# Kernel tuning notes

Hardware: AMD Instinct MI355X
Metric: run time of the kernel (lower is better)

Reference implementation:

```python
import jax, jax.numpy as jnp
import numpy as np

K = 20  # neighbors, per get_u_xt default


def setup_inputs() -> dict:
    key = jax.random.key(0)
    ks = jax.random.split(key, 6)
    B, N, D, H = 2048, 100000, 64, 256
    return {
        "t": jax.random.uniform(ks[0], (1,), dtype=jnp.float32),
        "z": jax.random.normal(ks[1], (B, D + 2), dtype=jnp.float32),
        "data": jax.random.normal(ks[2], (N, D), dtype=jnp.float32),
        "velocity": jax.random.normal(ks[3], (N, D), dtype=jnp.float32),
        "W1": jax.random.normal(ks[4], (D + 1, H), dtype=jnp.float32) * 0.05,
        "b1": jnp.zeros((H,), dtype=jnp.float32),
        "W2": jax.random.normal(ks[5], (H, D), dtype=jnp.float32) * 0.05,
        "b2": jnp.zeros((D,), dtype=jnp.float32),
    }


def _get_u_xt(xt, x, v, k=K):
    # Euclidean cdist via ||a||^2 + ||b||^2 - 2 a.b  -> [B, N]
    sq = (jnp.sum(xt * xt, axis=1)[:, None]
          + jnp.sum(x * x, axis=1)[None, :]
          - 2.0 * (xt @ x.T))
    dists = jnp.sqrt(jnp.maximum(sq, 1e-30))
    neg_d, knn_idx = jax.lax.top_k(-dists, k)  # k smallest distances
    knn_dists = -neg_d                          # ascending order, [B, k]
    h = jnp.maximum(knn_dists[:, -1:], 1e-12)   # bandwidth = k-th NN dist
    w = jnp.exp(-knn_dists ** 2 / (2.0 * h ** 2))
    w = w / (jnp.sum(w, axis=1, keepdims=True) + 1e-12)
    v_knn = v[knn_idx]                          # gather [B, k, D]
    return jnp.einsum('bk,bkd->bd', w, v_knn)


def reference(t, z, data, velocity, W1, b1, W2, b2):
    x = z[:, :-2]                               # [B, D]
    B = x.shape[0]
    inp = jnp.concatenate([x, jnp.broadcast_to(t, (B,))[:, None]], axis=1)
    x_dot = jax.nn.relu(inp @ W1 + b1) @ W2 + b2  # MLP model(...) -> [B, D]
    u_t = _get_u_xt(x, data, velocity)
    eps = 1e-8  # torch F.cosine_similarity eps
    nu = jnp.maximum(jnp.linalg.norm(u_t, axis=1), eps)
    nx = jnp.maximum(jnp.linalg.norm(x_dot, axis=1), eps)
    cos_sim = 1.0 - jnp.sum(u_t * x_dot, axis=1) / (nu * nx)
    L2_squared = jnp.sum((u_t - x_dot) ** 2, axis=1)
    return jnp.concatenate([x_dot, cos_sim[:, None], L2_squared[:, None]], axis=1)
```

## Files before the change

### kernel.cpp

```cpp
#include <hip/hip_runtime.h>
#include <math.h>

#define B      2048
#define N      100000
#define NPAD2  100352
#define JGRP   49
#define JT3    16
#define DD     64
#define HH     256
#define KK     20
#define SAMPLE 4096
#define CAP    1536
#define SSEL   512
#define SLACK  1.5f
#define LCAP   32

#define INF_F (__builtin_inff())

typedef __bf16 bf16x8 __attribute__((ext_vector_type(8)));
typedef __bf16 bf16x4 __attribute__((ext_vector_type(4)));
typedef float  floatx4 __attribute__((ext_vector_type(4)));
union U16 { uint4 u; bf16x8 v; };

__device__ __forceinline__ float wsum64(float v) {
    #pragma unroll
    for (int o = 32; o > 0; o >>= 1) v += __shfl_xor(v, o, 64);
    return v;
}

__global__ __launch_bounds__(64) void prep_kernel(const float* __restrict__ z,
                                                  float* __restrict__ xs,
                                                  float* __restrict__ xnorm,
                                                  __bf16* __restrict__ xs_h,
                                                  int* __restrict__ cnt) {
    int b = blockIdx.x, d = threadIdx.x;
    float v = z[b * 66 + d];
    xs[b * 64 + d] = v;
    xs_h[b * 64 + d] = (__bf16)v;
    float s = wsum64(v * v);
    if (d == 0) xnorm[b] = s;
    if (d == 1) cnt[b] = 0;
}

__global__ __launch_bounds__(256) void data_prep(const float* __restrict__ data,
                                                 float* __restrict__ dnorm,
                                                 float* __restrict__ dnh,
                                                 __bf16* __restrict__ d_hi) {
    int gt = blockIdx.x * 256 + threadIdx.x;
    int j = gt >> 4;
    int l = gt & 15;
    if (j >= NPAD2) return;
    float4 v = make_float4(0.f, 0.f, 0.f, 0.f);
    if (j < N)
        v = reinterpret_cast<const float4*>(data + (size_t)j * 64)[l];
    bf16x4 o;
    o.x = (__bf16)v.x; o.y = (__bf16)v.y; o.z = (__bf16)v.z; o.w = (__bf16)v.w;
    *reinterpret_cast<bf16x4*>(d_hi + (size_t)j * 64 + l * 4) = o;
    float s = v.x * v.x + v.y * v.y + v.z * v.z + v.w * v.w;
    #pragma unroll
    for (int o2 = 1; o2 < 16; o2 <<= 1) s += __shfl_xor(s, o2, 64);
    if (l == 0) {
        dnorm[j] = (j < N) ? s : INF_F;
        dnh[j]   = (j < N) ? 0.5f * s : INF_F;
    }
}

__global__ __launch_bounds__(256) void mlp_kernel(const float* __restrict__ z,
                                                  const float* __restrict__ tp,
                                                  const float* __restrict__ W1,
                                                  const float* __restrict__ b1,
                                                  const float* __restrict__ W2,
                                                  const float* __restrict__ b2,
                                                  float* __restrict__ xdot) {
    __shared__ float sin_[8][65];
    __shared__ float shid[8][HH];
    int tid = threadIdx.x;
    int row0 = blockIdx.x * 8;
    float tval = tp[0];
    for (int idx = tid; idx < 8 * 64; idx += 256) {
        int r = idx >> 6, d = idx & 63;
        sin_[r][d] = z[(row0 + r) * 66 + d];
    }
    if (tid < 8) sin_[tid][64] = tval;
    __syncthreads();

    int h = tid;
    float acc[8];
    #pragma unroll
    for (int r = 0; r < 8; ++r) acc[r] = b1[h];
    for (int i = 0; i < 65; ++i) {
        float wv = W1[i * HH + h];
        #pragma unroll
        for (int r = 0; r < 8; ++r) acc[r] = fmaf(sin_[r][i], wv, acc[r]);
    }
    #pragma unroll
    for (int r = 0; r < 8; ++r) shid[r][h] = fmaxf(acc[r], 0.f);
    __syncthreads();

    int d = tid & 63, rb = tid >> 6;
    for (int rr = rb; rr < 8; rr += 4) {
        float a = b2[d];
        #pragma unroll 8
        for (int hh2 = 0; hh2 < HH; ++hh2)
            a = fmaf(shid[rr][hh2], W2[hh2 * 64 + d], a);
        xdot[(size_t)(row0 + rr) * 64 + d] = a;
    }
}

__global__ __launch_bounds__(256) void sample_gemm(const __bf16* __restrict__ xs_h,
                                                   const __bf16* __restrict__ d_hi,
                                                   const float* __restrict__ xnorm,
                                                   const float* __restrict__ dnorm,
                                                   float* __restrict__ samp) {
    int tid = threadIdx.x;
    int m0 = blockIdx.x * 128;
    int jbase = blockIdx.y * 128;
    int wv = tid >> 6, wm = wv & 1, wn = wv >> 1;
    int lane = tid & 63, l16 = lane & 15, quad = lane >> 4;

    bf16x8 af[2][4], bfr[2][4];
    #pragma unroll
    for (int s = 0; s < 2; ++s)
        #pragma unroll
        for (int mt = 0; mt < 4; ++mt) {
            int row = m0 + wm * 64 + mt * 16 + l16;
            U16 u; u.u = reinterpret_cast<const uint4*>(xs_h + (size_t)row * 64)[s * 4 + quad];
            af[s][mt] = u.v;
        }
    #pragma unroll
    for (int s = 0; s < 2; ++s)
        #pragma unroll
        for (int nt = 0; nt < 4; ++nt) {
            int jr = jbase + wn * 64 + nt * 16 + l16;
            U16 u; u.u = reinterpret_cast<const uint4*>(d_hi + (size_t)jr * 64)[s * 4 + quad];
            bfr[s][nt] = u.v;
        }
    float dn[4], sxn[4][4];
    #pragma unroll
    for (int nt = 0; nt < 4; ++nt)
        dn[nt] = dnorm[jbase + wn * 64 + nt * 16 + l16];
    #pragma unroll
    for (int mt = 0; mt < 4; ++mt)
        #pragma unroll
        for (int rg = 0; rg < 4; ++rg)
            sxn[mt][rg] = xnorm[m0 + wm * 64 + mt * 16 + quad * 4 + rg];

    floatx4 acc[4][4];
    #pragma unroll
    for (int mt = 0; mt < 4; ++mt)
        #pragma unroll
        for (int nt = 0; nt < 4; ++nt)
            acc[mt][nt] = (floatx4){0.f, 0.f, 0.f, 0.f};
    #pragma unroll
    for (int s = 0; s < 2; ++s)
        #pragma unroll
        for (int mt = 0; mt < 4; ++mt)
            #pragma unroll
            for (int nt = 0; nt < 4; ++nt)
                acc[mt][nt] = __builtin_amdgcn_mfma_f32_16x16x32_bf16(
                    af[s][mt], bfr[s][nt], acc[mt][nt], 0, 0, 0);

    #pragma unroll
    for (int mt = 0; mt < 4; ++mt)
        #pragma unroll
        for (int nt = 0; nt < 4; ++nt) {
            floatx4 a4 = acc[mt][nt];
            int j = jbase + wn * 64 + nt * 16 + l16;
            #pragma unroll
            for (int rg = 0; rg < 4; ++rg) {
                int row = m0 + wm * 64 + mt * 16 + quad * 4 + rg;
                samp[(size_t)row * SAMPLE + j] = fmaf(a4[rg], -2.f, dn[nt]) + sxn[mt][rg];
            }
        }
}

__global__ __launch_bounds__(256) void thr_select(const float* __restrict__ samp,
                                                  float* __restrict__ thr) {
    __shared__ unsigned keys[SAMPLE];
    __shared__ int hist[256];
    __shared__ int s_bin, s_rank;
    int row = blockIdx.x, tid = threadIdx.x;
    for (int i = tid; i < SAMPLE; i += 256)
        keys[i] = __float_as_uint(fmaxf(samp[(size_t)row * SAMPLE + i], 0.f));
    int rank = KK - 1;
    unsigned prefix = 0, pmask = 0;
    for (int round = 0; round < 4; ++round) {
        int shift = 24 - 8 * round;
        hist[tid] = 0;
        __syncthreads();
        for (int i = tid; i < SAMPLE; i += 256) {
            unsigned k = keys[i];
            if ((k & pmask) == prefix) atomicAdd(&hist[(k >> shift) & 255], 1);
        }
        __syncthreads();
        if (tid < 64) {
            int base = tid * 4;
            int h0 = hist[base], h1 = hist[base + 1], h2 = hist[base + 2], h3 = hist[base + 3];
            int s4 = h0 + h1 + h2 + h3;
            int incl = s4;
            #pragma unroll
            for (int o = 1; o < 64; o <<= 1) {
                int t = __shfl_up(incl, o, 64);
                if (tid >= o) incl += t;
            }
            int excl = incl - s4;
            if (rank >= excl && rank < incl) {
                int r = rank - excl; int b = 0;
                if (r >= h0) { r -= h0; b = 1;
                    if (r >= h1) { r -= h1; b = 2;
                        if (r >= h2) { r -= h2; b = 3; } } }
                s_bin = base + b; s_rank = r;
            }
        }
        __syncthreads();
        prefix |= ((unsigned)s_bin) << shift;
        pmask  |= 0xFFu << shift;
        rank = s_rank;
    }
    if (tid == 0) thr[row] = __uint_as_float(prefix);
}

__global__ __launch_bounds__(256, 2) void gemm_filter(const __bf16* __restrict__ xs_h,
                                                      const __bf16* __restrict__ d_hi,
                                                      const float* __restrict__ xnorm,
                                                      const float* __restrict__ dnh,
                                                      const float* __restrict__ thr,
                                                      int* __restrict__ cnt,
                                                      float* __restrict__ bufd,
                                                      int* __restrict__ bufi) {
    __shared__ float sc[128];
    __shared__ float sts[128];
    __shared__ int   lcnt[128];
    __shared__ float lbd[128][LCAP + 1];
    __shared__ int   lbj[128][LCAP + 1];
    int tid = threadIdx.x;
    int m0 = blockIdx.x * 128;
    int jstart = blockIdx.y * (JT3 * 128);
    int wv = tid >> 6, wm = wv & 1, wn = wv >> 1;
    int lane = tid & 63, l16 = lane & 15, quad = lane >> 4;

    if (tid < 128) {
        float t2 = thr[m0 + tid] + 2.0f * SLACK;
        sts[tid] = t2;
        sc[tid] = 0.5f * (t2 - xnorm[m0 + tid]);
        lcnt[tid] = 0;
    }
    bf16x8 af[2][4];
    #pragma unroll
    for (int s = 0; s < 2; ++s)
        #pragma unroll
        for (int mt = 0; mt < 4; ++mt) {
            int row = m0 + wm * 64 + mt * 16 + l16;
            U16 u; u.u = reinterpret_cast<const uint4*>(xs_h + (size_t)row * 64)[s * 4 + quad];
            af[s][mt] = u.v;
        }
    __syncthreads();

    uint4 bb[2][8];
    float dh[2][4];
    {
        int jb = jstart;
        #pragma unroll
        for (int s = 0; s < 2; ++s)
            #pragma unroll
            for (int nt = 0; nt < 4; ++nt) {
                int jr = jb + wn * 64 + nt * 16 + l16;
                bb[0][s * 4 + nt] = reinterpret_cast<const uint4*>(d_hi + (size_t)jr * 64)[s * 4 + quad];
            }
        #pragma unroll
        for (int nt = 0; nt < 4; ++nt)
            dh[0][nt] = dnh[jb + wn * 64 + nt * 16 + l16];
    }

    #pragma unroll 2
    for (int t = 0; t < JT3; ++t) {
        int cur = t & 1, nxt = cur ^ 1;
        if (t + 1 < JT3) {
            int jb = jstart + (t + 1) * 128;
            #pragma unroll
            for (int s = 0; s < 2; ++s)
                #pragma unroll
                for (int nt = 0; nt < 4; ++nt) {
                    int jr = jb + wn * 64 + nt * 16 + l16;
                    bb[nxt][s * 4 + nt] = reinterpret_cast<const uint4*>(d_hi + (size_t)jr * 64)[s * 4 + quad];
                }
            #pragma unroll
            for (int nt = 0; nt < 4; ++nt)
                dh[nxt][nt] = dnh[jb + wn * 64 + nt * 16 + l16];
        }

        floatx4 acc[4][4];
        #pragma unroll
        for (int mt = 0; mt < 4; ++mt) {
            float4 cv = *reinterpret_cast<const float4*>(&sc[wm * 64 + mt * 16 + quad * 4]);
            #pragma unroll
            for (int nt = 0; nt < 4; ++nt)
                acc[mt][nt] = (floatx4){cv.x, cv.y, cv.z, cv.w};
        }
        #pragma unroll
        for (int s = 0; s < 2; ++s)
            #pragma unroll
            for (int mt = 0; mt < 4; ++mt)
                #pragma unroll
                for (int nt = 0; nt < 4; ++nt) {
                    U16 u; u.u = bb[cur][s * 4 + nt];
                    acc[mt][nt] = __builtin_amdgcn_mfma_f32_16x16x32_bf16(
                        af[s][mt], u.v, acc[mt][nt], 0, 0, 0);
                }

        int jb = jstart + t * 128;
        #pragma unroll
        for (int nt = 0; nt < 4; ++nt) {
            int nloc = wn * 64 + nt * 16 + l16;
            int j = jb + nloc;
            float dd = dh[cur][nt];
            #pragma unroll
            for (int mt = 0; mt < 4; ++mt) {
                floatx4 a4 = acc[mt][nt];
                bool p0 = a4[0] >= dd, p1 = a4[1] >= dd;
                bool p2 = a4[2] >= dd, p3 = a4[3] >= dd;
                if (p0 | p1 | p2 | p3) {
                    #pragma unroll
                    for (int rg = 0; rg < 4; ++rg) {
                        bool pp = (rg == 0) ? p0 : (rg == 1) ? p1 : (rg == 2) ? p2 : p3;
                        if (pp) {
                            int mloc = wm * 64 + mt * 16 + quad * 4 + rg;
                            float delta = 2.0f * (dd - a4[rg]);
                            int pos = atomicAdd(&lcnt[mloc], 1);
                            if (pos < LCAP) {
                                lbd[mloc][pos] = delta;
                                lbj[mloc][pos] = j;
                            } else {
                                int row = m0 + mloc;
                                int gp = atomicAdd(&cnt[row], 1);
                                if (gp < CAP) {
                                    bufd[(size_t)row * CAP + gp] = sts[mloc] + delta;
                                    bufi[(size_t)row * CAP + gp] = j;
                                }
                            }
                        }
                    }
                }
            }
        }
    }
    __syncthreads();
    if (tid < 128) {
        int c = lcnt[tid];
        if (c > LCAP) c = LCAP;
        if (c > 0) {
            int row = m0 + tid;
            float ts = sts[tid];
            int base = atomicAdd(&cnt[row], c);
            for (int i = 0; i < c; ++i) {
                int gp = base + i;
                if (gp < CAP) {
                    bufd[(size_t)row * CAP + gp] = ts + lbd[tid][i];
                    bufi[(size_t)row * CAP + gp] = lbj[tid][i];
                }
            }
        }
    }
}

__global__ __launch_bounds__(64) void select_finish(const float* __restrict__ bufd,
                                                    const int* __restrict__ bufi,
                                                    const int* __restrict__ cnt,
                                                    const float* __restrict__ xs,
                                                    const float* __restrict__ xnorm,
                                                    const float* __restrict__ dnorm,
                                                    const float* __restrict__ data,
                                                    const float* __restrict__ xdot,
                                                    const float* __restrict__ vel,
                                                    float* __restrict__ out) {
    __shared__ float sd[CAP];
    __shared__ int   si[CAP];
    __shared__ float sx[64];
    __shared__ float se[SSEL];
    __shared__ int   sj[SSEL];
    __shared__ int   hist[256];
    __shared__ int   s_bin, s_rank, scnt;
    __shared__ float seld[KK];
    __shared__ int   seli[KK];
    __shared__ float selw[KK];
    int row = blockIdx.x, lane = threadIdx.x;
    int n = cnt[row];
    if (n > CAP) n = CAP;
    for (int i = lane; i < n; i += 64) {
        sd[i] = bufd[(size_t)row * CAP + i];
        si[i] = bufi[(size_t)row * CAP + i];
    }
    sx[lane] = xs[row * 64 + lane];
    if (lane == 0) scnt = 0;
    __syncthreads();

    int rank = KK - 1;
    unsigned prefix = 0, pmask = 0;
    for (int round = 0; round < 4; ++round) {
        int shift = 24 - 8 * round;
        #pragma unroll
        for (int i = 0; i < 4; ++i) hist[lane + i * 64] = 0;
        __syncthreads();
        for (int i = lane; i < n; i += 64) {
            unsigned k = __float_as_uint(fmaxf(sd[i], 0.f));
            if ((k & pmask) == prefix) atomicAdd(&hist[(k >> shift) & 255], 1);
        }
        __syncthreads();
        {
            int base = lane * 4;
            int h0 = hist[base], h1 = hist[base + 1], h2 = hist[base + 2], h3 = hist[base + 3];
            int s4 = h0 + h1 + h2 + h3;
            int incl = s4;
            #pragma unroll
            for (int o = 1; o < 64; o <<= 1) {
                int t = __shfl_up(incl, o, 64);
                if (lane >= o) incl += t;
            }
            int excl = incl - s4;
            if (rank >= excl && rank < incl) {
                int r = rank - excl; int b = 0;
                if (r >= h0) { r -= h0; b = 1;
                    if (r >= h1) { r -= h1; b = 2;
                        if (r >= h2) { r -= h2; b = 3; } } }
                s_bin = base + b; s_rank = r;
            }
        }
        __syncthreads();
        prefix |= ((unsigned)s_bin) << shift;
        pmask  |= 0xFFu << shift;
        rank = s_rank;
    }
    float T = __uint_as_float(prefix);

    for (int i = lane; i < n; i += 64) {
        if (sd[i] <= T + 2.0f * SLACK) {
            int q = atomicAdd(&scnt, 1);
            if (q < SSEL) sj[q] = si[i];
        }
    }
    __syncthreads();
    int m = scnt < SSEL ? scnt : SSEL;
    for (int c = lane; c < m; c += 64) {
        int j = sj[c];
        const float4* dp = reinterpret_cast<const float4*>(data + (size_t)j * 64);
        float dot = 0.f;
        #pragma unroll
        for (int kb = 0; kb < 16; ++kb) {
            float4 q = dp[kb];
            dot = fmaf(sx[kb * 4 + 0], q.x, dot);
            dot = fmaf(sx[kb * 4 + 1], q.y, dot);
            dot = fmaf(sx[kb * 4 + 2], q.z, dot);
            dot = fmaf(sx[kb * 4 + 3], q.w, dot);
        }
        se[c] = xnorm[row] + dnorm[j] - 2.0f * dot;
    }
    __syncthreads();
    for (int k = 0; k < KK; ++k) {
        float v = INF_F; int id = 0x7fffffff; int p = -1;
        for (int i = lane; i < m; i += 64) {
            float x = se[i]; int xi = sj[i];
            if (x < v || (x == v && xi < id)) { v = x; id = xi; p = i; }
        }
        #pragma unroll
        for (int o = 32; o > 0; o >>= 1) {
            float ov = __shfl_xor(v, o, 64);
            int oid = __shfl_xor(id, o, 64);
            int op  = __shfl_xor(p, o, 64);
            if (ov < v || (ov == v && oid < id)) { v = ov; id = oid; p = op; }
        }
        if (lane == 0) {
            seld[k] = v; seli[k] = id;
            if (p >= 0) se[p] = INF_F;
        }
        __syncthreads();
    }
    float d20 = sqrtf(fmaxf(seld[KK - 1], 1e-30f));
    float h = fmaxf(d20, 1e-12f);
    float wk = 0.f;
    if (lane < KK) {
        float dd = sqrtf(fmaxf(seld[lane], 1e-30f));
        wk = expf(-(dd * dd) / (2.f * h * h));
    }
    float tot = wsum64(wk) + 1e-12f;
    if (lane < KK) selw[lane] = wk / tot;
    __syncthreads();
    float u = 0.f;
    #pragma unroll
    for (int k = 0; k < KK; ++k)
        u = fmaf(selw[k], vel[(size_t)seli[k] * 64 + lane], u);
    float xd = xdot[(size_t)row * 64 + lane];
    float du  = wsum64(u * xd);
    float nu2 = wsum64(u * u);
    float nx2 = wsum64(xd * xd);
    float l2  = wsum64((u - xd) * (u - xd));
    float nu = fmaxf(sqrtf(nu2), 1e-8f);
    float nx = fmaxf(sqrtf(nx2), 1e-8f);
    out[(size_t)row * 66 + lane] = xd;
    if (lane == 0) {
        out[(size_t)row * 66 + 64] = 1.f - du / (nu * nx);
        out[(size_t)row * 66 + 65] = l2;
    }
}

extern "C" void kernel_launch(void* const* d_in, const int* in_sizes, int n_in,
                              void* d_out, int out_size, void* d_ws, size_t ws_size,
                              hipStream_t stream) {
    const float* t_   = (const float*)d_in[0];
    const float* z    = (const float*)d_in[1];
    const float* data = (const float*)d_in[2];
    const float* vel  = (const float*)d_in[3];
    const float* W1   = (const float*)d_in[4];
    const float* b1   = (const float*)d_in[5];
    const float* W2   = (const float*)d_in[6];
    const float* b2   = (const float*)d_in[7];
    float* out = (float*)d_out;

    float*  xs    = (float*)d_ws;
    float*  xnorm = xs + 131072;
    float*  thr   = xnorm + 2048;
    int*    cnt   = (int*)(thr + 2048);
    float*  xdot  = (float*)(cnt + 2048);
    float*  dnorm = xdot + 131072;
    float*  dnh   = dnorm + NPAD2;
    __bf16* xs_h  = (__bf16*)(dnh + NPAD2);
    __bf16* d_hi  = xs_h + 131072;
    float*  samp  = (float*)(d_hi + (size_t)NPAD2 * 64);
    float*  bufd  = samp;
    int*    bufi  = (int*)(bufd + (size_t)B * CAP);

    prep_kernel<<<B, 64, 0, stream>>>(z, xs, xnorm, xs_h, cnt);
    data_prep<<<(NPAD2 * 16) / 256, 256, 0, stream>>>(data, dnorm, dnh, d_hi);
    mlp_kernel<<<B / 8, 256, 0, stream>>>(z, t_, W1, b1, W2, b2, xdot);
    sample_gemm<<<dim3(B / 128, SAMPLE / 128), 256, 0, stream>>>(xs_h, d_hi, xnorm, dnorm, samp);
    thr_select<<<B, 256, 0, stream>>>(samp, thr);
    gemm_filter<<<dim3(B / 128, JGRP), 256, 0, stream>>>(
        xs_h, d_hi, xnorm, dnh, thr, cnt, bufd, bufi);
    select_finish<<<B, 64, 0, stream>>>(bufd, bufi, cnt, xs, xnorm, dnorm, data,
                                        xdot, vel, out);
    (void)ws_size; (void)in_sizes; (void)n_in; (void)out_size;
}
```

Before: 346.7 us.

## Fuse setup kernels, compress sample to 16-bit keys, bitwise threshold search

Merges the data prep, row prep and MLP kernels into one launch split by block index. The sample distance matrix is doubled to 8192 columns but stored as truncated 16-bit float keys, and the threshold is found with a per-wave bitwise binary search held in registers instead of shared-memory radix histograms. The filter GEMM uses narrower 64-column tiles over twice as many groups, with per-row constants kept in registers and a higher occupancy hint. The finishing kernel's radix select is also replaced with a bitwise search. Together these aim to cut launch count, sample traffic and selection overhead, at the cost of a coarser threshold and a smaller candidate buffer that could overflow.

```diff
diff --git a/kernel.cpp b/kernel.cpp
--- a/kernel.cpp
+++ b/kernel.cpp
@@ -4,16 +4,16 @@
 #define B      2048
 #define N      100000
 #define NPAD2  100352
-#define JGRP   49
-#define JT3    16
+#define JGRP2  98
+#define JT4    16
 #define DD     64
 #define HH     256
 #define KK     20
-#define SAMPLE 4096
-#define CAP    1536
+#define SAMPLE 8192
+#define CAP    1024
 #define SSEL   512
 #define SLACK  1.5f
-#define LCAP   32
+#define LCAP   16
 
 #define INF_F (__builtin_inff())
 
@@ -27,83 +27,87 @@
     for (int o = 32; o > 0; o >>= 1) v += __shfl_xor(v, o, 64);
     return v;
 }
-
-__global__ __launch_bounds__(64) void prep_kernel(const float* __restrict__ z,
-                                                  float* __restrict__ xs,
-                                                  float* __restrict__ xnorm,
-                                                  __bf16* __restrict__ xs_h,
-                                                  int* __restrict__ cnt) {
-    int b = blockIdx.x, d = threadIdx.x;
-    float v = z[b * 66 + d];
-    xs[b * 64 + d] = v;
-    xs_h[b * 64 + d] = (__bf16)v;
-    float s = wsum64(v * v);
-    if (d == 0) xnorm[b] = s;
-    if (d == 1) cnt[b] = 0;
-}
-
-__global__ __launch_bounds__(256) void data_prep(const float* __restrict__ data,
+__device__ __forceinline__ int wsum64i(int v) {
+    #pragma unroll
+    for (int o = 32; o > 0; o >>= 1) v += __shfl_xor(v, o, 64);
+    return v;
+}
+
+#define NB_DATA 6272
+#define NB_PREP 512
+#define NB_MLP  256
+__global__ __launch_bounds__(256) void setup_all(const float* __restrict__ z,
+                                                 const float* __restrict__ tp,
+                                                 const float* __restrict__ data,
+                                                 const float* __restrict__ W1,
+                                                 const float* __restrict__ b1,
+                                                 const float* __restrict__ W2,
+                                                 const float* __restrict__ b2,
+                                                 float* __restrict__ xs,
+                                                 float* __restrict__ xnorm,
+                                                 __bf16* __restrict__ xs_h,
+                                                 int* __restrict__ cnt,
                                                  float* __restrict__ dnorm,
                                                  float* __restrict__ dnh,
-                                                 __bf16* __restrict__ d_hi) {
-    int gt = blockIdx.x * 256 + threadIdx.x;
-    int j = gt >> 4;
-    int l = gt & 15;
-    if (j >= NPAD2) return;
-    float4 v = make_float4(0.f, 0.f, 0.f, 0.f);
-    if (j < N)
-        v = reinterpret_cast<const float4*>(data + (size_t)j * 64)[l];
-    bf16x4 o;
-    o.x = (__bf16)v.x; o.y = (__bf16)v.y; o.z = (__bf16)v.z; o.w = (__bf16)v.w;
-    *reinterpret_cast<bf16x4*>(d_hi + (size_t)j * 64 + l * 4) = o;
-    float s = v.x * v.x + v.y * v.y + v.z * v.z + v.w * v.w;
-    #pragma unroll
-    for (int o2 = 1; o2 < 16; o2 <<= 1) s += __shfl_xor(s, o2, 64);
-    if (l == 0) {
-        dnorm[j] = (j < N) ? s : INF_F;
-        dnh[j]   = (j < N) ? 0.5f * s : INF_F;
-    }
-}
-
-__global__ __launch_bounds__(256) void mlp_kernel(const float* __restrict__ z,
-                                                  const float* __restrict__ tp,
-                                                  const float* __restrict__ W1,
-                                                  const float* __restrict__ b1,
-                                                  const float* __restrict__ W2,
-                                                  const float* __restrict__ b2,
-                                                  float* __restrict__ xdot) {
-    __shared__ float sin_[8][65];
-    __shared__ float shid[8][HH];
-    int tid = threadIdx.x;
-    int row0 = blockIdx.x * 8;
-    float tval = tp[0];
-    for (int idx = tid; idx < 8 * 64; idx += 256) {
-        int r = idx >> 6, d = idx & 63;
-        sin_[r][d] = z[(row0 + r) * 66 + d];
-    }
-    if (tid < 8) sin_[tid][64] = tval;
-    __syncthreads();
-
-    int h = tid;
-    float acc[8];
-    #pragma unroll
-    for (int r = 0; r < 8; ++r) acc[r] = b1[h];
-    for (int i = 0; i < 65; ++i) {
-        float wv = W1[i * HH + h];
-        #pragma unroll
-        for (int r = 0; r < 8; ++r) acc[r] = fmaf(sin_[r][i], wv, acc[r]);
-    }
-    #pragma unroll
-    for (int r = 0; r < 8; ++r) shid[r][h] = fmaxf(acc[r], 0.f);
-    __syncthreads();
-
-    int d = tid & 63, rb = tid >> 6;
-    for (int rr = rb; rr < 8; rr += 4) {
-        float a = b2[d];
-        #pragma unroll 8
-        for (int hh2 = 0; hh2 < HH; ++hh2)
-            a = fmaf(shid[rr][hh2], W2[hh2 * 64 + d], a);
-        xdot[(size_t)(row0 + rr) * 64 + d] = a;
+                                                 __bf16* __restrict__ d_hi,
+                                                 float* __restrict__ xdot) {
+    int bx = blockIdx.x, tid = threadIdx.x;
+    if (bx < NB_DATA) {
+        int gt = bx * 256 + tid;
+        int j = gt >> 4, l = gt & 15;
+        float4 v = make_float4(0.f, 0.f, 0.f, 0.f);
+        if (j < N)
+            v = reinterpret_cast<const float4*>(data + (size_t)j * 64)[l];
+        bf16x4 o;
+        o.x = (__bf16)v.x; o.y = (__bf16)v.y; o.z = (__bf16)v.z; o.w = (__bf16)v.w;
+        *reinterpret_cast<bf16x4*>(d_hi + (size_t)j * 64 + l * 4) = o;
+        float s = v.x * v.x + v.y * v.y + v.z * v.z + v.w * v.w;
+        #pragma unroll
+        for (int o2 = 1; o2 < 16; o2 <<= 1) s += __shfl_xor(s, o2, 64);
+        if (l == 0) {
+            dnorm[j] = (j < N) ? s : INF_F;
+            dnh[j]   = (j < N) ? 0.5f * s : INF_F;
+        }
+    } else if (bx < NB_DATA + NB_PREP) {
+        int row = (bx - NB_DATA) * 4 + (tid >> 6);
+        int d = tid & 63;
+        float v = z[row * 66 + d];
+        xs[row * 64 + d] = v;
+        xs_h[row * 64 + d] = (__bf16)v;
+        float s = wsum64(v * v);
+        if (d == 0) xnorm[row] = s;
+        if (d == 1) cnt[row] = 0;
+    } else {
+        __shared__ float sin_[8][65];
+        __shared__ float shid[8][HH];
+        int row0 = (bx - NB_DATA - NB_PREP) * 8;
+        float tval = tp[0];
+        for (int idx = tid; idx < 8 * 64; idx += 256) {
+            int r = idx >> 6, d = idx & 63;
+            sin_[r][d] = z[(row0 + r) * 66 + d];
+        }
+        if (tid < 8) sin_[tid][64] = tval;
+        __syncthreads();
+        int h = tid;
+        float acc[8];
+        #pragma unroll
+        for (int r = 0; r < 8; ++r) acc[r] = b1[h];
+        for (int i = 0; i < 65; ++i) {
+            float wv = W1[i * HH + h];
+            #pragma unroll
+            for (int r = 0; r < 8; ++r) acc[r] = fmaf(sin_[r][i], wv, acc[r]);
+        }
+        #pragma unroll
+        for (int r = 0; r < 8; ++r) shid[r][h] = fmaxf(acc[r], 0.f);
+        __syncthreads();
+        int d = tid & 63, rb = tid >> 6;
+        for (int rr = rb; rr < 8; rr += 4) {
+            float a = b2[d];
+            #pragma unroll 8
+            for (int hh2 = 0; hh2 < HH; ++hh2)
+                a = fmaf(shid[rr][hh2], W2[hh2 * 64 + d], a);
+            xdot[(size_t)(row0 + rr) * 64 + d] = a;
+        }
     }
 }
 
@@ -111,7 +115,7 @@
                                                    const __bf16* __restrict__ d_hi,
                                                    const float* __restrict__ xnorm,
                                                    const float* __restrict__ dnorm,
-                                                   float* __restrict__ samp) {
+                                                   unsigned short* __restrict__ samp16) {
     int tid = threadIdx.x;
     int m0 = blockIdx.x * 128;
     int jbase = blockIdx.y * 128;
@@ -169,58 +173,37 @@
             #pragma unroll
             for (int rg = 0; rg < 4; ++rg) {
                 int row = m0 + wm * 64 + mt * 16 + quad * 4 + rg;
-                samp[(size_t)row * SAMPLE + j] = fmaf(a4[rg], -2.f, dn[nt]) + sxn[mt][rg];
+                float sq = fmaf(a4[rg], -2.f, dn[nt]) + sxn[mt][rg];
+                samp16[(size_t)row * SAMPLE + j] =
+                    (unsigned short)(__float_as_uint(fmaxf(sq, 0.f)) >> 16);
             }
         }
 }
 
-__global__ __launch_bounds__(256) void thr_select(const float* __restrict__ samp,
+__global__ __launch_bounds__(256) void thr_select(const unsigned short* __restrict__ samp16,
                                                   float* __restrict__ thr) {
-    __shared__ unsigned keys[SAMPLE];
-    __shared__ int hist[256];
-    __shared__ int s_bin, s_rank;
-    int row = blockIdx.x, tid = threadIdx.x;
-    for (int i = tid; i < SAMPLE; i += 256)
-        keys[i] = __float_as_uint(fmaxf(samp[(size_t)row * SAMPLE + i], 0.f));
-    int rank = KK - 1;
-    unsigned prefix = 0, pmask = 0;
-    for (int round = 0; round < 4; ++round) {
-        int shift = 24 - 8 * round;
-        hist[tid] = 0;
-        __syncthreads();
-        for (int i = tid; i < SAMPLE; i += 256) {
-            unsigned k = keys[i];
-            if ((k & pmask) == prefix) atomicAdd(&hist[(k >> shift) & 255], 1);
-        }
-        __syncthreads();
-        if (tid < 64) {
-            int base = tid * 4;
-            int h0 = hist[base], h1 = hist[base + 1], h2 = hist[base + 2], h3 = hist[base + 3];
-            int s4 = h0 + h1 + h2 + h3;
-            int incl = s4;
-            #pragma unroll
-            for (int o = 1; o < 64; o <<= 1) {
-                int t = __shfl_up(incl, o, 64);
-                if (tid >= o) incl += t;
-            }
-            int excl = incl - s4;
-            if (rank >= excl && rank < incl) {
-                int r = rank - excl; int b = 0;
-                if (r >= h0) { r -= h0; b = 1;
-                    if (r >= h1) { r -= h1; b = 2;
-                        if (r >= h2) { r -= h2; b = 3; } } }
-                s_bin = base + b; s_rank = r;
-            }
-        }
-        __syncthreads();
-        prefix |= ((unsigned)s_bin) << shift;
-        pmask  |= 0xFFu << shift;
-        rank = s_rank;
-    }
-    if (tid == 0) thr[row] = __uint_as_float(prefix);
-}
-
-__global__ __launch_bounds__(256, 2) void gemm_filter(const __bf16* __restrict__ xs_h,
+    int wv = threadIdx.x >> 6, lane = threadIdx.x & 63;
+    int row = blockIdx.x * 4 + wv;
+    const unsigned* sp = reinterpret_cast<const unsigned*>(samp16 + (size_t)row * SAMPLE);
+    unsigned w[64];
+    #pragma unroll
+    for (int i = 0; i < 64; ++i) w[i] = sp[lane + i * 64];
+    unsigned res = 0;
+    for (int b = 15; b >= 0; --b) {
+        unsigned cand = res | (1u << b);
+        int c = 0;
+        #pragma unroll
+        for (int i = 0; i < 64; ++i) {
+            c += ((w[i] & 0xFFFFu) < cand);
+            c += ((w[i] >> 16) < cand);
+        }
+        c = wsum64i(c);
+        if (c <= KK - 1) res = cand;
+    }
+    if (lane == 0) thr[row] = __uint_as_float((res + 1u) << 16);
+}
+
+__global__ __launch_bounds__(256, 3) void gemm_filter(const __bf16* __restrict__ xs_h,
                                                       const __bf16* __restrict__ d_hi,
                                                       const float* __restrict__ xnorm,
                                                       const float* __restrict__ dnh,
@@ -228,21 +211,18 @@
                                                       int* __restrict__ cnt,
                                                       float* __restrict__ bufd,
                                                       int* __restrict__ bufi) {
-    __shared__ float sc[128];
     __shared__ float sts[128];
     __shared__ int   lcnt[128];
     __shared__ float lbd[128][LCAP + 1];
     __shared__ int   lbj[128][LCAP + 1];
     int tid = threadIdx.x;
     int m0 = blockIdx.x * 128;
-    int jstart = blockIdx.y * (JT3 * 128);
+    int jstart = blockIdx.y * (JT4 * 64);
     int wv = tid >> 6, wm = wv & 1, wn = wv >> 1;
     int lane = tid & 63, l16 = lane & 15, quad = lane >> 4;
 
     if (tid < 128) {
-        float t2 = thr[m0 + tid] + 2.0f * SLACK;
-        sts[tid] = t2;
-        sc[tid] = 0.5f * (t2 - xnorm[m0 + tid]);
+        sts[tid] = thr[m0 + tid] + 2.0f * SLACK;
         lcnt[tid] = 0;
     }
     bf16x8 af[2][4];
@@ -254,65 +234,71 @@
             U16 u; u.u = reinterpret_cast<const uint4*>(xs_h + (size_t)row * 64)[s * 4 + quad];
             af[s][mt] = u.v;
         }
-    __syncthreads();
-
-    uint4 bb[2][8];
-    float dh[2][4];
+    float scv[4][4];
+    #pragma unroll
+    for (int mt = 0; mt < 4; ++mt)
+        #pragma unroll
+        for (int rg = 0; rg < 4; ++rg) {
+            int mg = m0 + wm * 64 + mt * 16 + quad * 4 + rg;
+            scv[mt][rg] = 0.5f * (thr[mg] + 2.0f * SLACK - xnorm[mg]);
+        }
+    __syncthreads();
+
+    uint4 bb[2][4];
+    float dh[2][2];
     {
-        int jb = jstart;
         #pragma unroll
         for (int s = 0; s < 2; ++s)
             #pragma unroll
-            for (int nt = 0; nt < 4; ++nt) {
-                int jr = jb + wn * 64 + nt * 16 + l16;
-                bb[0][s * 4 + nt] = reinterpret_cast<const uint4*>(d_hi + (size_t)jr * 64)[s * 4 + quad];
+            for (int nt = 0; nt < 2; ++nt) {
+                int jr = jstart + wn * 32 + nt * 16 + l16;
+                bb[0][s * 2 + nt] = reinterpret_cast<const uint4*>(d_hi + (size_t)jr * 64)[s * 4 + quad];
             }
         #pragma unroll
-        for (int nt = 0; nt < 4; ++nt)
-            dh[0][nt] = dnh[jb + wn * 64 + nt * 16 + l16];
+        for (int nt = 0; nt < 2; ++nt)
+            dh[0][nt] = dnh[jstart + wn * 32 + nt * 16 + l16];
     }
 
     #pragma unroll 2
-    for (int t = 0; t < JT3; ++t) {
+    for (int t = 0; t < JT4; ++t) {
         int cur = t & 1, nxt = cur ^ 1;
-        if (t + 1 < JT3) {
-            int jb = jstart + (t + 1) * 128;
+        if (t + 1 < JT4) {
+            int jb = jstart + (t + 1) * 64;
             #pragma unroll
             for (int s = 0; s < 2; ++s)
                 #pragma unroll
-                for (int nt = 0; nt < 4; ++nt) {
-                    int jr = jb + wn * 64 + nt * 16 + l16;
-                    bb[nxt][s * 4 + nt] = reinterpret_cast<const uint4*>(d_hi + (size_t)jr * 64)[s * 4 + quad];
+                for (int nt = 0; nt < 2; ++nt) {
+                    int jr = jb + wn * 32 + nt * 16 + l16;
+                    bb[nxt][s * 2 + nt] = reinterpret_cast<const uint4*>(d_hi + (size_t)jr * 64)[s * 4 + quad];
                 }
             #pragma unroll
-            for (int nt = 0; nt < 4; ++nt)
-                dh[nxt][nt] = dnh[jb + wn * 64 + nt * 16 + l16];
-        }
-
-        floatx4 acc[4][4];
+            for (int nt = 0; nt < 2; ++nt)
+                dh[nxt][nt] = dnh[jb + wn * 32 + nt * 16 + l16];
+        }
+
+        floatx4 acc[4][2];
         #pragma unroll
         for (int mt = 0; mt < 4; ++mt) {
-            float4 cv = *reinterpret_cast<const float4*>(&sc[wm * 64 + mt * 16 + quad * 4]);
-            #pragma unroll
-            for (int nt = 0; nt < 4; ++nt)
-                acc[mt][nt] = (floatx4){cv.x, cv.y, cv.z, cv.w};
-        }
-        #pragma unroll
-        for (int s = 0; s < 2; ++s)
-            #pragma unroll
-            for (int mt = 0; mt < 4; ++mt)
-                #pragma unroll
-                for (int nt = 0; nt < 4; ++nt) {
-                    U16 u; u.u = bb[cur][s * 4 + nt];
-                    acc[mt][nt] = __builtin_amdgcn_mfma_f32_16x16x32_bf16(
-                        af[s][mt], u.v, acc[mt][nt], 0, 0, 0);
-                }
-
-        int jb = jstart + t * 128;
-        #pragma unroll
-        for (int nt = 0; nt < 4; ++nt) {
-            int nloc = wn * 64 + nt * 16 + l16;
-            int j = jb + nloc;
+            floatx4 cv = (floatx4){scv[mt][0], scv[mt][1], scv[mt][2], scv[mt][3]};
+            acc[mt][0] = cv;
+            acc[mt][1] = cv;
+        }
+        #pragma unroll
+        for (int s = 0; s < 2; ++s) {
+            U16 u0, u1;
+            u0.u = bb[cur][s * 2 + 0];
+            u1.u = bb[cur][s * 2 + 1];
+            #pragma unroll
+            for (int mt = 0; mt < 4; ++mt) {
+                acc[mt][0] = __builtin_amdgcn_mfma_f32_16x16x32_bf16(af[s][mt], u0.v, acc[mt][0], 0, 0, 0);
+                acc[mt][1] = __builtin_amdgcn_mfma_f32_16x16x32_bf16(af[s][mt], u1.v, acc[mt][1], 0, 0, 0);
+            }
+        }
+
+        int jb = jstart + t * 64;
+        #pragma unroll
+        for (int nt = 0; nt < 2; ++nt) {
+            int j = jb + wn * 32 + nt * 16 + l16;
             float dd = dh[cur][nt];
             #pragma unroll
             for (int mt = 0; mt < 4; ++mt) {
@@ -378,8 +364,7 @@
     __shared__ float sx[64];
     __shared__ float se[SSEL];
     __shared__ int   sj[SSEL];
-    __shared__ int   hist[256];
-    __shared__ int   s_bin, s_rank, scnt;
+    __shared__ int   scnt;
     __shared__ float seld[KK];
     __shared__ int   seli[KK];
     __shared__ float selw[KK];
@@ -394,43 +379,16 @@
     if (lane == 0) scnt = 0;
     __syncthreads();
 
-    int rank = KK - 1;
-    unsigned prefix = 0, pmask = 0;
-    for (int round = 0; round < 4; ++round) {
-        int shift = 24 - 8 * round;
-        #pragma unroll
-        for (int i = 0; i < 4; ++i) hist[lane + i * 64] = 0;
-        __syncthreads();
-        for (int i = lane; i < n; i += 64) {
-            unsigned k = __float_as_uint(fmaxf(sd[i], 0.f));
-            if ((k & pmask) == prefix) atomicAdd(&hist[(k >> shift) & 255], 1);
-        }
-        __syncthreads();
-        {
-            int base = lane * 4;
-            int h0 = hist[base], h1 = hist[base + 1], h2 = hist[base + 2], h3 = hist[base + 3];
-            int s4 = h0 + h1 + h2 + h3;
-            int incl = s4;
-            #pragma unroll
-            for (int o = 1; o < 64; o <<= 1) {
-                int t = __shfl_up(incl, o, 64);
-                if (lane >= o) incl += t;
-            }
-            int excl = incl - s4;
-            if (rank >= excl && rank < incl) {
-                int r = rank - excl; int b = 0;
-                if (r >= h0) { r -= h0; b = 1;
-                    if (r >= h1) { r -= h1; b = 2;
-                        if (r >= h2) { r -= h2; b = 3; } } }
-                s_bin = base + b; s_rank = r;
-            }
-        }
-        __syncthreads();
-        prefix |= ((unsigned)s_bin) << shift;
-        pmask  |= 0xFFu << shift;
-        rank = s_rank;
-    }
-    float T = __uint_as_float(prefix);
+    unsigned res = 0;
+    for (int b = 30; b >= 0; --b) {
+        unsigned cand = res | (1u << b);
+        int c = 0;
+        for (int i = lane; i < n; i += 64)
+            c += (__float_as_uint(fmaxf(sd[i], 0.f)) < cand);
+        c = wsum64i(c);
+        if (c <= KK - 1) res = cand;
+    }
+    float T = __uint_as_float(res);
 
     for (int i = lane; i < n; i += 64) {
         if (sd[i] <= T + 2.0f * SLACK) {
@@ -524,16 +482,15 @@
     float*  dnh   = dnorm + NPAD2;
     __bf16* xs_h  = (__bf16*)(dnh + NPAD2);
     __bf16* d_hi  = xs_h + 131072;
-    float*  samp  = (float*)(d_hi + (size_t)NPAD2 * 64);
-    float*  bufd  = samp;
+    unsigned short* samp16 = (unsigned short*)(d_hi + (size_t)NPAD2 * 64);
+    float*  bufd  = (float*)samp16;
     int*    bufi  = (int*)(bufd + (size_t)B * CAP);
 
-    prep_kernel<<<B, 64, 0, stream>>>(z, xs, xnorm, xs_h, cnt);
-    data_prep<<<(NPAD2 * 16) / 256, 256, 0, stream>>>(data, dnorm, dnh, d_hi);
-    mlp_kernel<<<B / 8, 256, 0, stream>>>(z, t_, W1, b1, W2, b2, xdot);
-    sample_gemm<<<dim3(B / 128, SAMPLE / 128), 256, 0, stream>>>(xs_h, d_hi, xnorm, dnorm, samp);
-    thr_select<<<B, 256, 0, stream>>>(samp, thr);
-    gemm_filter<<<dim3(B / 128, JGRP), 256, 0, stream>>>(
+    setup_all<<<NB_DATA + NB_PREP + NB_MLP, 256, 0, stream>>>(
+        z, t_, data, W1, b1, W2, b2, xs, xnorm, xs_h, cnt, dnorm, dnh, d_hi, xdot);
+    sample_gemm<<<dim3(B / 128, SAMPLE / 128), 256, 0, stream>>>(xs_h, d_hi, xnorm, dnorm, samp16);
+    thr_select<<<B / 4, 256, 0, stream>>>(samp16, thr);
+    gemm_filter<<<dim3(B / 128, JGRP2), 256, 0, stream>>>(
         xs_h, d_hi, xnorm, dnh, thr, cnt, bufd, bufi);
     select_finish<<<B, 64, 0, stream>>>(bufd, bufi, cnt, xs, xnorm, dnorm, data,
                                         xdot, vel, out);
```

Measured after the change: 299.5 us. 1.16x faster.
